# Kernel tuning notes

Hardware: AMD Instinct MI355X
Metric: run time of the kernel (lower is better)

## Reference

```python
import jax, jax.numpy as jnp
import numpy as np

CONF_THRESH = 0.25
IOU_THRESH = 0.45
MAX_PER_IMG = 100
K_PRE = 512          # fixed pre-NMS candidate count (padding for jit)
CLS_OFFSET = 4096.0  # class offset for non-class-agnostic NMS (torchvision batched_nms trick)


def setup_inputs() -> dict:
    key = jax.random.key(0)
    k1, k2, k3, k4 = jax.random.split(key, 4)
    B, N, C = 32, 8400, 80
    # YOLOX raw output layout: (cx, cy, w, h, obj, cls_0..cls_C-1)
    cxcy = jax.random.uniform(k1, (B, N, 2), dtype=jnp.float32) * 640.0
    wh = jax.random.uniform(k2, (B, N, 2), dtype=jnp.float32) * 128.0 + 4.0
    obj = jax.random.uniform(k3, (B, N, 1), dtype=jnp.float32)
    cls = jax.random.uniform(k4, (B, N, C), dtype=jnp.float32)
    pred = jnp.concatenate([cxcy, wh, obj, cls], axis=-1)  # [B, N, 85]
    return {"pred": pred}


def _pairwise_iou(b):
    # b: [K, 4] xyxy -> [K, K] IoU
    x1 = jnp.maximum(b[:, None, 0], b[None, :, 0])
    y1 = jnp.maximum(b[:, None, 1], b[None, :, 1])
    x2 = jnp.minimum(b[:, None, 2], b[None, :, 2])
    y2 = jnp.minimum(b[:, None, 3], b[None, :, 3])
    inter = jnp.clip(x2 - x1, 0.0) * jnp.clip(y2 - y1, 0.0)
    area = (b[:, 2] - b[:, 0]) * (b[:, 3] - b[:, 1])
    union = area[:, None] + area[None, :] - inter
    return inter / (union + 1e-9)


def _nms(boxes, valid):
    # boxes [K,4] already sorted by score desc; valid [K] bool. Greedy NMS.
    iou = _pairwise_iou(boxes)

    def body(i, keep):
        # keep[j] is False for j >= i, so this only checks earlier kept boxes
        suppressed = jnp.any(keep & (iou[i] > IOU_THRESH))
        return keep.at[i].set(valid[i] & jnp.logical_not(suppressed))

    return jax.lax.fori_loop(0, K_PRE, body, jnp.zeros(K_PRE, dtype=bool))


def reference(pred):
    # --- box decode: cxcywh -> xyxy (YOLOX postprocess box_corner) ---
    half = pred[..., 2:4] * 0.5
    boxes = jnp.concatenate([pred[..., :2] - half, pred[..., :2] + half], axis=-1)  # [B,N,4]
    obj = pred[..., 4]                 # [B,N]
    cls = pred[..., 5:]                # [B,N,C]
    class_conf = cls.max(axis=-1)      # [B,N]
    class_pred = jnp.argmax(cls, axis=-1)  # [B,N] int
    scores = obj * class_conf          # [B,N]

    # per-image adaptive conf: min(conf_thresh, best score) -> at least 1 survives
    conf = jnp.minimum(CONF_THRESH, scores.max(axis=-1, keepdims=True))  # [B,1]
    valid = scores >= conf
    masked = jnp.where(valid, scores, -jnp.inf)

    # fixed-size candidate set, sorted by score desc
    top_scores, idx = jax.lax.top_k(masked, K_PRE)  # [B,K]
    b_k = jnp.take_along_axis(boxes, idx[..., None], axis=1)       # [B,K,4]
    obj_k = jnp.take_along_axis(obj, idx, axis=1)                  # [B,K]
    cc_k = jnp.take_along_axis(class_conf, idx, axis=1)            # [B,K]
    cp_k = jnp.take_along_axis(class_pred, idx, axis=1)            # [B,K]
    valid_k = jnp.isfinite(top_scores)

    # class_agnostic=False: offset boxes by class so cross-class IoU is 0
    nms_boxes = b_k + cp_k.astype(b_k.dtype)[..., None] * CLS_OFFSET
    keep = jax.vmap(_nms)(nms_boxes, valid_k)  # [B,K] bool

    # compact kept boxes to the front (stable argsort preserves score order)
    order = jnp.argsort(jnp.where(keep, jnp.arange(K_PRE), K_PRE), axis=-1)
    sel = order[:, :MAX_PER_IMG]                                   # [B,M]
    mask = jnp.take_along_axis(keep, sel, axis=1)                  # [B,M]

    dets = jnp.concatenate(
        [b_k, obj_k[..., None], cc_k[..., None], cp_k.astype(b_k.dtype)[..., None]],
        axis=-1,
    )  # [B,K,7] = (x1,y1,x2,y2,obj,class_conf,class_pred)
    dets = jnp.take_along_axis(dets, sel[..., None], axis=1)       # [B,M,7]
    dets = dets * mask[..., None].astype(dets.dtype)
    return dets, mask
```

## Files before the change

### kernel.cpp

```cpp
#include <hip/hip_runtime.h>

#define NB 32
#define NN 8400
#define NC 80
#define KPRE 512
#define MAXOUT 100
#define NGRP 263
#define NWV 526

__global__ __launch_bounds__(128) void score_kernel(const float* __restrict__ pred,
                                                    float* __restrict__ scores,
                                                    unsigned* __restrict__ wmaxg,
                                                    float4* __restrict__ rawbox,
                                                    float4* __restrict__ minfo) {
    int b = blockIdx.y;
    int w = threadIdx.x >> 6, lane = threadIdx.x & 63;
    int g = blockIdx.x * 2 + w;
    __shared__ float4 stg4[2][340];
    const float4* p4 = (const float4*)pred;
    size_t base4 = (size_t)b * 178500 + (size_t)g * 340;
    size_t img_end4 = ((size_t)b + 1) * 178500;
    for (int k = lane; k < 340; k += 64) {
        size_t e = base4 + k;
        if (e >= img_end4) e = img_end4 - 1;
        stg4[w][k] = p4[e];
    }
    int rl = lane >> 2, q = lane & 3;
    int row = g * 16 + rl;
    const float* r = (const float*)&stg4[w][0] + rl * 85;
    float cx = r[0], cy = r[1], bw = r[2], bh = r[3], obj = r[4];
    int c0 = 5 + q * 20;
    float cc = r[c0];
    int cp = q * 20;
    for (int c = 1; c < 20; c++) {
        float v = r[c0 + c];
        if (v > cc) { cc = v; cp = q * 20 + c; }
    }
    {
        float cc1 = __shfl_xor(cc, 1, 64); int cp1 = __shfl_xor(cp, 1, 64);
        bool take = (cc1 > cc) || (cc1 == cc && cp1 < cp);
        cc = take ? cc1 : cc; cp = take ? cp1 : cp;
        float cc2 = __shfl_xor(cc, 2, 64); int cp2 = __shfl_xor(cp, 2, 64);
        take = (cc2 > cc) || (cc2 == cc && cp2 < cp);
        cc = take ? cc2 : cc; cp = take ? cp2 : cp;
    }
    float s = __fmul_rn(obj, cc);
    float hw = __fmul_rn(bw, 0.5f), hh = __fmul_rn(bh, 0.5f);
    float x1 = cx - hw, y1 = cy - hh, x2 = cx + hw, y2 = cy + hh;
    int srcl = (lane & 15) * 4;
    float v0 = __shfl(x1, srcl, 64);
    float v1 = __shfl(y1, srcl, 64);
    float v2 = __shfl(x2, srcl, 64);
    float v3 = __shfl(y2, srcl, 64);
    float v4 = __shfl(obj, srcl, 64);
    float v5 = __shfl(cc, srcl, 64);
    int   v6 = __shfl(cp, srcl, 64);
    float v7 = __shfl(s, srcl, 64);
    int wrow = g * 16 + (lane & 15);
    if (lane < 16 && wrow < NN) {
        size_t idx = (size_t)b * NN + wrow;
        scores[idx] = v7;
        rawbox[idx] = make_float4(v0, v1, v2, v3);
        minfo[idx]  = make_float4(v4, v5, (float)v6, v7);
    }
    if (row >= NN) s = 0.0f;
    unsigned bits = __float_as_uint(s);
    for (int o = 32; o > 0; o >>= 1) {
        unsigned other = (unsigned)__shfl_down((int)bits, o, 64);
        if (other > bits) bits = other;
    }
    if (lane == 0) wmaxg[b * NWV + g] = bits;
}

__device__ __forceinline__ void find_bin(const unsigned* hist, int cstart, unsigned T, int lane,
                                         int* outB, unsigned* outR) {
    unsigned running = 0;
    unsigned v = hist[cstart * 64 + lane];
    for (int c = cstart; c >= 0; c--) {
        unsigned vn = (c > 0) ? hist[(c - 1) * 64 + lane] : 0u;
        unsigned s = v;
        for (int off = 1; off < 64; off <<= 1) {
            unsigned u = (unsigned)__shfl_down((int)s, off, 64);
            if (lane + off < 64) s += u;
        }
        unsigned total0 = (unsigned)__shfl((int)s, 0, 64);
        if (total0 + running >= T) {
            unsigned long long mask = __ballot(s + running >= T);
            int m = 63 - __clzll(mask);
            unsigned sm = (unsigned)__shfl((int)s, m, 64);
            unsigned vm = (unsigned)__shfl((int)v, m, 64);
            if (lane == 0) { *outB = c * 64 + m; *outR = T - (sm + running - vm); }
            return;
        }
        running += total0;
        v = vn;
    }
    if (lane == 0) { *outB = 0; *outR = T; }
}

__global__ __launch_bounds__(1024) void selnms_kernel(const float* __restrict__ scores,
                                                      const unsigned* __restrict__ wmaxg,
                                                      const float4* __restrict__ rawbox,
                                                      const float4* __restrict__ minfo,
                                                      float* __restrict__ out) {
    int b = blockIdx.x, t = threadIdx.x;
    int lane = t & 63;
    __shared__ unsigned histA[2048];
    __shared__ unsigned histB[2048];
    __shared__ unsigned long long list[KPRE];
    __shared__ unsigned long long sorted[KPRE];
    __shared__ unsigned long long elist64[256];
    __shared__ int srank[KPRE];
    __shared__ float4 sb[KPRE];
    __shared__ float4 sraw[KPRE];
    __shared__ float4 smeta[KPRE];
    __shared__ float  sarea[KPRE];
    __shared__ unsigned long long siou[KPRE * 8];
    __shared__ unsigned long long skeep[8];
    __shared__ int S_B[2];
    __shared__ unsigned S_T[2];
    __shared__ int S_cnt, S_ecnt, S_done;
    __shared__ float S_conf;
    __shared__ unsigned S_mbits;

    if (t == 0) { S_cnt = 0; S_ecnt = 0; S_done = 0; }
    if (t < 64) {
        unsigned tmp[9];
#pragma unroll
        for (int k = 0; k < 9; k++) {
            int i = t + k * 64;
            tmp[k] = (i < NWV) ? wmaxg[b * NWV + i] : 0u;
        }
        unsigned m = 0;
#pragma unroll
        for (int k = 0; k < 9; k++) if (tmp[k] > m) m = tmp[k];
        for (int off = 32; off > 0; off >>= 1) {
            unsigned o = (unsigned)__shfl_down((int)m, off, 64);
            if (o > m) m = o;
        }
        if (t == 0) { S_conf = fminf(0.25f, __uint_as_float(m)); S_mbits = m; }
    }
    for (int i = t; i < 2048; i += 1024) { histA[i] = 0; histB[i] = 0; }
    for (int i = t; i < KPRE * 8; i += 1024) siou[i] = 0ull;
    if (t < 256) elist64[t] = 0ull;
    __syncthreads();
    float conf = S_conf;
    const float4* sc4 = (const float4*)(scores + (size_t)b * NN);
    unsigned ka[8];
    unsigned kb[4] = {0u, 0u, 0u, 0u};
    {
        float4 u0 = sc4[2 * t], u1 = sc4[2 * t + 1];
        ka[0] = (u0.x >= conf) ? __float_as_uint(u0.x) : 0u;
        ka[1] = (u0.y >= conf) ? __float_as_uint(u0.y) : 0u;
        ka[2] = (u0.z >= conf) ? __float_as_uint(u0.z) : 0u;
        ka[3] = (u0.w >= conf) ? __float_as_uint(u0.w) : 0u;
        ka[4] = (u1.x >= conf) ? __float_as_uint(u1.x) : 0u;
        ka[5] = (u1.y >= conf) ? __float_as_uint(u1.y) : 0u;
        ka[6] = (u1.z >= conf) ? __float_as_uint(u1.z) : 0u;
        ka[7] = (u1.w >= conf) ? __float_as_uint(u1.w) : 0u;
        if (t < 52) {
            float4 u2 = sc4[2048 + t];
            kb[0] = (u2.x >= conf) ? __float_as_uint(u2.x) : 0u;
            kb[1] = (u2.y >= conf) ? __float_as_uint(u2.y) : 0u;
            kb[2] = (u2.z >= conf) ? __float_as_uint(u2.z) : 0u;
            kb[3] = (u2.w >= conf) ? __float_as_uint(u2.w) : 0u;
        }
#pragma unroll
        for (int j = 0; j < 8; j++) atomicAdd(&histA[ka[j] >> 21], 1u);
        if (t < 52) {
#pragma unroll
            for (int j = 0; j < 4; j++) atomicAdd(&histA[kb[j] >> 21], 1u);
        }
    }
    __syncthreads();
    if (t < 64) {
        int cs = (int)(S_mbits >> 27); if (cs > 31) cs = 31;
        find_bin(histA, cs, 512u, t, &S_B[0], &S_T[0]);
    }
    __syncthreads();
    int B1 = S_B[0]; unsigned R1 = S_T[0];
#pragma unroll
    for (int j = 0; j < 8; j++) {
        unsigned k = ka[j];
        if ((int)(k >> 21) == B1) atomicAdd(&histB[(k >> 10) & 0x7FFu], 1u);
    }
    if (t < 52) {
#pragma unroll
        for (int j = 0; j < 4; j++) {
            unsigned k = kb[j];
            if ((int)(k >> 21) == B1) atomicAdd(&histB[(k >> 10) & 0x7FFu], 1u);
        }
    }
    __syncthreads();
    if (t < 64) find_bin(histB, 31, R1, t, &S_B[1], &S_T[1]);
    __syncthreads();
    unsigned P = ((unsigned)B1 << 11) | (unsigned)S_B[1];
    unsigned R2 = S_T[1];
    unsigned long long ltmask = (1ull << lane) - 1ull;
#pragma unroll
    for (int j = 0; j < 8; j++) {
        unsigned k = ka[j];
        unsigned n = 8u * (unsigned)t + (unsigned)j;
        unsigned long long key = ((unsigned long long)k << 32) | (unsigned long long)(unsigned)(~n);
        bool win = (k >> 10) > P;
        bool tie = (P != 0u) && ((k >> 10) == P);
        unsigned long long mw = __ballot(win);
        unsigned long long mtie = __ballot(tie);
        int baseW = 0, baseT = 0;
        if (lane == 0) {
            if (mw)   baseW = atomicAdd(&S_cnt, __popcll(mw));
            if (mtie) baseT = atomicAdd(&S_ecnt, __popcll(mtie));
        }
        baseW = __shfl(baseW, 0, 64);
        baseT = __shfl(baseT, 0, 64);
        if (win) {
            list[baseW + __popcll(mw & ltmask)] = key;
        } else if (tie) {
            int ep = baseT + __popcll(mtie & ltmask);
            if (ep < 256) elist64[ep] = key;
        }
    }
    if (t < 52) {
#pragma unroll
        for (int j = 0; j < 4; j++) {
            unsigned k = kb[j];
            unsigned n = 8192u + 4u * (unsigned)t + (unsigned)j;
            unsigned long long key = ((unsigned long long)k << 32) | (unsigned long long)(unsigned)(~n);
            bool win = (k >> 10) > P;
            bool tie = (P != 0u) && ((k >> 10) == P);
            unsigned long long mw = __ballot(win);
            unsigned long long mtie = __ballot(tie);
            int baseW = 0, baseT = 0;
            if (lane == 0) {
                if (mw)   baseW = atomicAdd(&S_cnt, __popcll(mw));
                if (mtie) baseT = atomicAdd(&S_ecnt, __popcll(mtie));
            }
            baseW = __shfl(baseW, 0, 64);
            baseT = __shfl(baseT, 0, 64);
            if (win) {
                list[baseW + __popcll(mw & ltmask)] = key;
            } else if (tie) {
                int ep = baseT + __popcll(mtie & ltmask);
                if (ep < 256) elist64[ep] = key;
            }
        }
    }
    __syncthreads();
    int ecnt = S_ecnt; if (ecnt > 256) ecnt = 256;
    if (t < ecnt) {
        unsigned long long my = elist64[t];
        const ulonglong2* e2 = (const ulonglong2*)elist64;
        int r = 0;
#pragma unroll 4
        for (int j = 0; j < 128; j += 4) {
            ulonglong2 a = e2[j], b2 = e2[j + 1], c2 = e2[j + 2], d2 = e2[j + 3];
            r += (int)(a.x > my) + (int)(a.y > my) + (int)(b2.x > my) + (int)(b2.y > my);
            r += (int)(c2.x > my) + (int)(c2.y > my) + (int)(d2.x > my) + (int)(d2.y > my);
        }
        if (r < (int)R2) {
            int pos = atomicAdd(&S_cnt, 1);
            list[pos] = my;
        }
    }
    __syncthreads();
    int nval = S_cnt;
    for (int i = nval + t; i < KPRE; i += 1024) list[i] = 0ull;
    __syncthreads();
    {
        int tt = t & 511, half = t >> 9;
        unsigned long long K0 = list[tt];
        const ulonglong2* l2 = (const ulonglong2*)list;
        int jb = half * 128;
        int r0 = 0;
#pragma unroll 4
        for (int j = 0; j < 128; j += 4) {
            ulonglong2 a = l2[jb + j], b2 = l2[jb + j + 1], c2 = l2[jb + j + 2], d2 = l2[jb + j + 3];
            r0 += (int)(a.x > K0) + (int)(a.y > K0) + (int)(b2.x > K0) + (int)(b2.y > K0);
            r0 += (int)(c2.x > K0) + (int)(c2.y > K0) + (int)(d2.x > K0) + (int)(d2.y > K0);
        }
        if (half) srank[tt] = r0;
        __syncthreads();
        if (!half) {
            int r = r0 + srank[tt];
            if (K0 != 0ull) sorted[r] = K0; else sorted[tt] = 0ull;
        }
    }
    __syncthreads();
    if (t < KPRE) {
        unsigned long long key = sorted[t];
        int valid = ((unsigned)(key >> 32)) != 0u;
        unsigned n = ~(unsigned)key;
        if (!valid) n = 0;
        size_t src = (size_t)b * NN + n;
        float4 rb = rawbox[src];
        float4 mi = minfo[src];
        float off = __fmul_rn(mi.z, 4096.0f);
        float4 bo = make_float4(rb.x + off, rb.y + off, rb.z + off, rb.w + off);
        sraw[t] = rb;
        sb[t] = bo;
        smeta[t] = make_float4(mi.x, mi.y, mi.z, valid ? 1.0f : 0.0f);
        sarea[t] = __fmul_rn(bo.z - bo.x, bo.w - bo.y);
    }
    __syncthreads();

    unsigned long long keepW = 0ull;
    int cnt = 0;
    int lg = t >> 3, lw = t & 7;
    int irow = t >> 4, iq = t & 15;

    for (int c = 0; c < 8; c++) {
        int row = (c << 6) + irow;
        float4 bi = sb[row];
        float ai = sarea[row];
        for (int k = 0; k <= c; k++) {
            unsigned long long wk = 0ull;
            int j0 = (k << 6) + iq;
#pragma unroll
            for (int s = 0; s < 4; s++) {
                int j = j0 + (s << 4);
                float4 bj = sb[j];
                float xx1 = fmaxf(bi.x, bj.x);
                float yy1 = fmaxf(bi.y, bj.y);
                float xx2 = fminf(bi.z, bj.z);
                float yy2 = fminf(bi.w, bj.w);
                float iw = fmaxf(xx2 - xx1, 0.0f);
                float ih = fmaxf(yy2 - yy1, 0.0f);
                float inter = __fmul_rn(iw, ih);
                float uni = (ai + sarea[j]) - inter;
                float iou = inter / (uni + 1e-9f);
                if (iou > 0.45f && j < row) wk |= 1ull << (j & 63);
            }
            if (wk) atomicOr(&siou[(row << 3) + k], wk);
        }
        __syncthreads();
        if (t < 64) {
            unsigned long long R[8];
#pragma unroll
            for (int k = 0; k < 8; k++) R[k] = siou[(c << 9) + (k << 6) + t];
#pragma unroll
            for (int k = 0; k < 8; k++) {
#pragma unroll
                for (int m = 0; m < 8; m++) {
                    int ii = (c << 6) + (k << 3) + m;
                    bool hit = (lg == m) && ((R[k] & keepW) != 0ull);
                    unsigned long long bal = __ballot(hit);
                    bool kept = (bal == 0ull) && (ii < nval);
                    if (kept) {
                        cnt++;
                        if (lw == c) keepW |= 1ull << ((k << 3) + m);
                    }
                }
            }
            if (t == 0) S_done = (cnt >= MAXOUT) ? 1 : 0;
        }
        __syncthreads();
        if (S_done) break;
    }
    if (t < 8) skeep[t] = keepW;
    __syncthreads();

    float* dets = out + (size_t)b * (MAXOUT * 7);
    float* maskp = out + (size_t)NB * MAXOUT * 7 + (size_t)b * MAXOUT;
    for (int m = t; m < MAXOUT * 7; m += 1024) dets[m] = 0.0f;
    for (int m = t; m < MAXOUT; m += 1024) maskp[m] = 0.0f;
    __syncthreads();
    if (t < KPRE) {
        int wq = t >> 6;
        unsigned long long kw = skeep[wq];
        if ((kw >> (t & 63)) & 1ull) {
            int rank = __popcll(kw & ((1ull << (t & 63)) - 1ull));
            for (int w2 = 0; w2 < wq; w2++) rank += __popcll(skeep[w2]);
            if (rank < MAXOUT) {
                float4 rb = sraw[t];
                float4 mt = smeta[t];
                float* rowp = dets + rank * 7;
                rowp[0] = rb.x; rowp[1] = rb.y; rowp[2] = rb.z; rowp[3] = rb.w;
                rowp[4] = mt.x; rowp[5] = mt.y; rowp[6] = mt.z;
                maskp[rank] = 1.0f;
            }
        }
    }
}

extern "C" void kernel_launch(void* const* d_in, const int* in_sizes, int n_in,
                              void* d_out, int out_size, void* d_ws, size_t ws_size,
                              hipStream_t stream) {
    const float* pred = (const float*)d_in[0];
    float* out = (float*)d_out;

    char* ws = (char*)d_ws;
    unsigned* wmaxg = (unsigned*)ws;
    float* scores = (float*)(ws + 67584);
    float4* rawbox = (float4*)(ws + 1142784);
    float4* minfo  = (float4*)(ws + 5443584);

    dim3 gA(NGRP, NB);
    score_kernel<<<gA, 128, 0, stream>>>(pred, scores, wmaxg, rawbox, minfo);
    selnms_kernel<<<NB, 1024, 0, stream>>>(scores, wmaxg, rawbox, minfo, out);
}
```

Baseline: 167.6 us.

## Replicate coarse histogram, skip zero keys, register-block rank sorts in selection kernel

The coarse score histogram becomes four interleaved copies stored in the siou buffer, and zero (below-threshold) keys skip the atomic, to cut atomic contention. The siou zeroing moves later, overlapping the second histogram pass. Both the tie-list and top-512 rank sorts now have each thread rank four keys per shared-memory read, which cuts LDS traffic, and the tie loop stops at the actual count. The cost is fewer active threads for the rank phase and extra register pressure.

```diff
diff --git a/kernel.cpp b/kernel.cpp
--- a/kernel.cpp
+++ b/kernel.cpp
@@ -98,6 +98,35 @@
     if (lane == 0) { *outB = 0; *outR = T; }
 }
 
+__device__ __forceinline__ void find_bin4(const uint4* h4, int cstart, unsigned T, int lane,
+                                          int* outB, unsigned* outR) {
+    unsigned running = 0;
+    uint4 q = h4[cstart * 64 + lane];
+    for (int c = cstart; c >= 0; c--) {
+        uint4 qn;
+        if (c > 0) qn = h4[(c - 1) * 64 + lane];
+        else { qn.x = 0; qn.y = 0; qn.z = 0; qn.w = 0; }
+        unsigned v = q.x + q.y + q.z + q.w;
+        unsigned s = v;
+        for (int off = 1; off < 64; off <<= 1) {
+            unsigned u = (unsigned)__shfl_down((int)s, off, 64);
+            if (lane + off < 64) s += u;
+        }
+        unsigned total0 = (unsigned)__shfl((int)s, 0, 64);
+        if (total0 + running >= T) {
+            unsigned long long mask = __ballot(s + running >= T);
+            int m = 63 - __clzll(mask);
+            unsigned sm = (unsigned)__shfl((int)s, m, 64);
+            unsigned vm = (unsigned)__shfl((int)v, m, 64);
+            if (lane == 0) { *outB = c * 64 + m; *outR = T - (sm + running - vm); }
+            return;
+        }
+        running += total0;
+        q = qn;
+    }
+    if (lane == 0) { *outB = 0; *outR = T; }
+}
+
 __global__ __launch_bounds__(1024) void selnms_kernel(const float* __restrict__ scores,
                                                       const unsigned* __restrict__ wmaxg,
                                                       const float4* __restrict__ rawbox,
@@ -105,12 +134,10 @@
                                                       float* __restrict__ out) {
     int b = blockIdx.x, t = threadIdx.x;
     int lane = t & 63;
-    __shared__ unsigned histA[2048];
     __shared__ unsigned histB[2048];
     __shared__ unsigned long long list[KPRE];
     __shared__ unsigned long long sorted[KPRE];
     __shared__ unsigned long long elist64[256];
-    __shared__ int srank[KPRE];
     __shared__ float4 sb[KPRE];
     __shared__ float4 sraw[KPRE];
     __shared__ float4 smeta[KPRE];
@@ -123,6 +150,9 @@
     __shared__ float S_conf;
     __shared__ unsigned S_mbits;
 
+    unsigned* histA4 = (unsigned*)siou;
+    int hcopy = (t >> 8) & 3;
+
     if (t == 0) { S_cnt = 0; S_ecnt = 0; S_done = 0; }
     if (t < 64) {
         unsigned tmp[9];
@@ -140,8 +170,8 @@
         }
         if (t == 0) { S_conf = fminf(0.25f, __uint_as_float(m)); S_mbits = m; }
     }
-    for (int i = t; i < 2048; i += 1024) { histA[i] = 0; histB[i] = 0; }
-    for (int i = t; i < KPRE * 8; i += 1024) siou[i] = 0ull;
+    for (int i = t; i < 8192; i += 1024) histA4[i] = 0;
+    for (int i = t; i < 2048; i += 1024) histB[i] = 0;
     if (t < 256) elist64[t] = 0ull;
     __syncthreads();
     float conf = S_conf;
@@ -166,16 +196,22 @@
             kb[3] = (u2.w >= conf) ? __float_as_uint(u2.w) : 0u;
         }
 #pragma unroll
-        for (int j = 0; j < 8; j++) atomicAdd(&histA[ka[j] >> 21], 1u);
+        for (int j = 0; j < 8; j++) {
+            unsigned k = ka[j];
+            if (k) atomicAdd(&histA4[((k >> 21) << 2) | hcopy], 1u);
+        }
         if (t < 52) {
 #pragma unroll
-            for (int j = 0; j < 4; j++) atomicAdd(&histA[kb[j] >> 21], 1u);
+            for (int j = 0; j < 4; j++) {
+                unsigned k = kb[j];
+                if (k) atomicAdd(&histA4[((k >> 21) << 2) | hcopy], 1u);
+            }
         }
     }
     __syncthreads();
     if (t < 64) {
         int cs = (int)(S_mbits >> 27); if (cs > 31) cs = 31;
-        find_bin(histA, cs, 512u, t, &S_B[0], &S_T[0]);
+        find_bin4((const uint4*)histA4, cs, 512u, t, &S_B[0], &S_T[0]);
     }
     __syncthreads();
     int B1 = S_B[0]; unsigned R1 = S_T[0];
@@ -191,6 +227,7 @@
             if ((int)(k >> 21) == B1) atomicAdd(&histB[(k >> 10) & 0x7FFu], 1u);
         }
     }
+    for (int i = t; i < KPRE * 8; i += 1024) siou[i] = 0ull;
     __syncthreads();
     if (t < 64) find_bin(histB, 31, R1, t, &S_B[1], &S_T[1]);
     __syncthreads();
@@ -246,43 +283,58 @@
         }
     }
     __syncthreads();
-    int ecnt = S_ecnt; if (ecnt > 256) ecnt = 256;
-    if (t < ecnt) {
-        unsigned long long my = elist64[t];
-        const ulonglong2* e2 = (const ulonglong2*)elist64;
-        int r = 0;
-#pragma unroll 4
-        for (int j = 0; j < 128; j += 4) {
-            ulonglong2 a = e2[j], b2 = e2[j + 1], c2 = e2[j + 2], d2 = e2[j + 3];
-            r += (int)(a.x > my) + (int)(a.y > my) + (int)(b2.x > my) + (int)(b2.y > my);
-            r += (int)(c2.x > my) + (int)(c2.y > my) + (int)(d2.x > my) + (int)(d2.y > my);
-        }
-        if (r < (int)R2) {
-            int pos = atomicAdd(&S_cnt, 1);
-            list[pos] = my;
+    {
+        int ecnt = S_ecnt; if (ecnt > 256) ecnt = 256;
+        if (t < 64 && 4 * t < ecnt) {
+            const ulonglong2* e2 = (const ulonglong2*)elist64;
+            ulonglong2 klo = e2[2 * t], khi = e2[2 * t + 1];
+            unsigned long long K[4] = { klo.x, klo.y, khi.x, khi.y };
+            int r[4] = {0, 0, 0, 0};
+            int jmax = (ecnt + 7) >> 3 << 2;
+#pragma unroll 1
+            for (int j = 0; j < jmax; j += 4) {
+                ulonglong2 a = e2[j], b2 = e2[j + 1], c2 = e2[j + 2], d2 = e2[j + 3];
+#pragma unroll
+                for (int q = 0; q < 4; q++) {
+                    r[q] += (int)(a.x > K[q]) + (int)(a.y > K[q])
+                          + (int)(b2.x > K[q]) + (int)(b2.y > K[q])
+                          + (int)(c2.x > K[q]) + (int)(c2.y > K[q])
+                          + (int)(d2.x > K[q]) + (int)(d2.y > K[q]);
+                }
+            }
+#pragma unroll
+            for (int q = 0; q < 4; q++) {
+                if (K[q] != 0ull && r[q] < (int)R2) {
+                    int pos = atomicAdd(&S_cnt, 1);
+                    list[pos] = K[q];
+                }
+            }
         }
     }
     __syncthreads();
     int nval = S_cnt;
     for (int i = nval + t; i < KPRE; i += 1024) list[i] = 0ull;
     __syncthreads();
-    {
-        int tt = t & 511, half = t >> 9;
-        unsigned long long K0 = list[tt];
+    if (t < 128) {
         const ulonglong2* l2 = (const ulonglong2*)list;
-        int jb = half * 128;
-        int r0 = 0;
-#pragma unroll 4
-        for (int j = 0; j < 128; j += 4) {
-            ulonglong2 a = l2[jb + j], b2 = l2[jb + j + 1], c2 = l2[jb + j + 2], d2 = l2[jb + j + 3];
-            r0 += (int)(a.x > K0) + (int)(a.y > K0) + (int)(b2.x > K0) + (int)(b2.y > K0);
-            r0 += (int)(c2.x > K0) + (int)(c2.y > K0) + (int)(d2.x > K0) + (int)(d2.y > K0);
-        }
-        if (half) srank[tt] = r0;
-        __syncthreads();
-        if (!half) {
-            int r = r0 + srank[tt];
-            if (K0 != 0ull) sorted[r] = K0; else sorted[tt] = 0ull;
+        ulonglong2 klo = l2[2 * t], khi = l2[2 * t + 1];
+        unsigned long long K[4] = { klo.x, klo.y, khi.x, khi.y };
+        int r[4] = {0, 0, 0, 0};
+#pragma unroll 1
+        for (int j = 0; j < 256; j += 4) {
+            ulonglong2 a = l2[j], b2 = l2[j + 1], c2 = l2[j + 2], d2 = l2[j + 3];
+#pragma unroll
+            for (int q = 0; q < 4; q++) {
+                r[q] += (int)(a.x > K[q]) + (int)(a.y > K[q])
+                      + (int)(b2.x > K[q]) + (int)(b2.y > K[q])
+                      + (int)(c2.x > K[q]) + (int)(c2.y > K[q])
+                      + (int)(d2.x > K[q]) + (int)(d2.y > K[q]);
+            }
+        }
+#pragma unroll
+        for (int q = 0; q < 4; q++) {
+            int p = 4 * t + q;
+            if (K[q] != 0ull) sorted[r[q]] = K[q]; else sorted[p] = 0ull;
         }
     }
     __syncthreads();
```

After: 170.9 us. No clear change (+2.0%).
